# Performance work log

Measured on AMD Instinct MI355X. Metric: run time of the kernel, lower is better.

The kernel has to match this reference:

```python
import jax, jax.numpy as jnp
import numpy as np

N, E = 20000, 320000
IN, H, C = 1024, 8, 64
HC = H * C
EDGE_DIM = 16
NUM_GRAPHS = 8
LEAKY_SLOPE = 0.2
LN_EPS = 1e-5


def setup_inputs() -> dict:
    key = jax.random.key(0)
    ks = jax.random.split(key, 12)
    s = 0.05
    return {
        "x": jax.random.normal(ks[0], (N, IN), jnp.float32),
        "edge_attr": jax.random.normal(ks[1], (E, EDGE_DIM), jnp.float32),
        "edge_index": jax.random.randint(ks[2], (2, E), 0, N, dtype=jnp.int64),
        "batch": jnp.sort(jax.random.randint(ks[3], (N,), 0, NUM_GRAPHS, dtype=jnp.int64)),
        "W_src": jax.random.normal(ks[4], (IN, HC), jnp.float32) * s,
        "W_dst": jax.random.normal(ks[5], (IN, HC), jnp.float32) * s,
        "att_src": jax.random.normal(ks[6], (H, C), jnp.float32) * s,
        "att_dst": jax.random.normal(ks[7], (H, C), jnp.float32) * s,
        "bias": jnp.zeros((HC,), jnp.float32),
        "ln_gamma": jnp.ones((HC,), jnp.float32),
        "ln_beta": jnp.zeros((HC,), jnp.float32),
        "prelu_a": jnp.full((HC,), 0.25, jnp.float32),
    }


def reference(x, edge_attr, edge_index, batch, W_src, W_dst, att_src, att_dst,
              bias, ln_gamma, ln_beta, prelu_a):
    # Eval mode: node/edge feature dropout and attention dropout are identity.
    # with_edge == 'N': edge_attr is unused by the conv.
    n = x.shape[0]
    src, dst = edge_index[0], edge_index[1]

    xs = (x @ W_src).reshape(n, H, C)   # source-side projections
    xd = (x @ W_dst).reshape(n, H, C)   # dest-side projections
    a_src = jnp.einsum('nhc,hc->nh', xs, att_src)
    a_dst = jnp.einsum('nhc,hc->nh', xd, att_dst)

    # edge scores + softmax over incoming edges of each destination node
    e = jax.nn.leaky_relu(a_src[src] + a_dst[dst], LEAKY_SLOPE)  # [E,H]
    m = jax.ops.segment_max(e, dst, num_segments=n)              # [N,H]
    m = jax.lax.stop_gradient(jnp.where(jnp.isfinite(m), m, 0.0))
    ex = jnp.exp(e - m[dst])
    denom = jax.ops.segment_sum(ex, dst, num_segments=n)
    alpha = ex / (denom[dst] + 1e-16)                            # [E,H]

    msg = alpha[:, :, None] * xs[src]                            # [E,H,C]
    out = jax.ops.segment_sum(msg, dst, num_segments=n).reshape(n, HC) + bias

    # norm_type == 'layer': the per-graph boolean-mask loop applies LayerNorm
    # row-wise; with sorted batch ids this equals a single LayerNorm over all
    # nodes (LayerNorm has no cross-row statistics).
    mu = jnp.mean(out, axis=-1, keepdims=True)
    var = jnp.mean(jnp.square(out - mu), axis=-1, keepdims=True)
    y = (out - mu) * jax.lax.rsqrt(var + LN_EPS) * ln_gamma + ln_beta

    # PReLU with per-channel slope
    return jnp.where(y >= 0, y, prelu_a * y)
```

## Files before the change

kernel.cpp:

```cpp
#include <hip/hip_runtime.h>
#include <hip/hip_bf16.h>

#define N_NODES 20000
#define N_EDGES 320000
#define IN_DIM  1024
#define H_HEADS 8
#define C_CH    64
#define HC      512
#define LEAKY   0.2f
#define LN_EPS  1e-5f

#define BCOLS 576

typedef short bf16x8 __attribute__((ext_vector_type(8)));
typedef float f32x4  __attribute__((ext_vector_type(4)));

__device__ __forceinline__ unsigned short f2bf(float f) {
    union { float f; unsigned int u; } c; c.f = f;
    unsigned int u = c.u;
    unsigned int r = (u + 0x7fffu + ((u >> 16) & 1u)) >> 16;
    return (unsigned short)r;
}
__device__ __forceinline__ float bf2f(unsigned int h) {
    union { unsigned int u; float f; } c; c.u = h << 16; return c.f;
}
__device__ __forceinline__ unsigned int bfpack(float lo, float hi) {
    return (unsigned int)f2bf(lo) | ((unsigned int)f2bf(hi) << 16);
}
__device__ __forceinline__ void gload_lds16(const void* g, void* l) {
    __builtin_amdgcn_global_load_lds(
        (const __attribute__((address_space(1))) unsigned int*)g,
        (__attribute__((address_space(3))) unsigned int*)l, 16, 0, 0);
}

#define DEG_BLOCKS 1250

__global__ __launch_bounds__(256) void deg_hist(
        const int* __restrict__ ei, int* __restrict__ deg) {
    int e = blockIdx.x * 256 + threadIdx.x;
    atomicAdd(&deg[ei[N_EDGES + e]], 1);
}

__global__ void prep_w_scan(const float* __restrict__ Wsrc,
                            const float* __restrict__ Wdst,
                            const float* __restrict__ att_src,
                            const float* __restrict__ att_dst,
                            short* __restrict__ wbT,
                            const int* __restrict__ deg,
                            int* __restrict__ off,
                            int* __restrict__ cursor) {
    int t = threadIdx.x;

    if (blockIdx.x == IN_DIM) {
        __shared__ int wtot[2];
        int lane = t & 63, w = t >> 6;
        const int4* deg4 = (const int4*)deg;
        int s = 0;
        if (t < 125) {
            #pragma unroll
            for (int j = 0; j < 40; ++j) {
                int4 u = deg4[t * 40 + j];
                s += u.x + u.y + u.z + u.w;
            }
        }
        int v = s;
        #pragma unroll
        for (int o = 1; o < 64; o <<= 1) {
            int u = __shfl_up(v, o);
            if (lane >= o) v += u;
        }
        if (lane == 63) wtot[w] = v;
        __syncthreads();
        int add = (w == 1) ? wtot[0] : 0;
        int run = add + v - s;
        if (t < 125) {
            int4* off4 = (int4*)off;
            int4* cur4 = (int4*)cursor;
            #pragma unroll
            for (int j = 0; j < 40; ++j) {
                int4 u = deg4[t * 40 + j];
                int4 o_;
                o_.x = run;
                o_.y = o_.x + u.x;
                o_.z = o_.y + u.y;
                o_.w = o_.z + u.z;
                off4[t * 40 + j] = o_;
                cur4[t * 40 + j] = o_;
                run = o_.w + u.w;
            }
            if (t == 124) off[N_NODES] = run;
        }
        return;
    }

    int k = blockIdx.x;
    float4 v = *(const float4*)(Wsrc + (size_t)k * HC + t * 4);
    wbT[(size_t)(t * 4 + 0) * IN_DIM + k] = (short)f2bf(v.x);
    wbT[(size_t)(t * 4 + 1) * IN_DIM + k] = (short)f2bf(v.y);
    wbT[(size_t)(t * 4 + 2) * IN_DIM + k] = (short)f2bf(v.z);
    wbT[(size_t)(t * 4 + 3) * IN_DIM + k] = (short)f2bf(v.w);
    if (t < 16) {
        int h = t & 7;
        const float* W   = (t < 8) ? Wsrc : Wdst;
        const float* att = (t < 8) ? att_src : att_dst;
        float s = 0.f;
        #pragma unroll
        for (int c = 0; c < C_CH; ++c)
            s += W[(size_t)k * HC + h * C_CH + c] * att[h * C_CH + c];
        wbT[(size_t)(512 + t) * IN_DIM + k] = (short)f2bf(s);
    } else if (t < 64) {
        wbT[(size_t)(512 + t) * IN_DIM + k] = 0;
    }
}

#define BM 64
#define BN 96
#define BK 64
#define NCOLT (BCOLS / BN)
#define NROWT ((N_NODES + BM - 1) / BM)
#define NWG (NCOLT * NROWT)
#define KSTEPS (IN_DIM / BK)
#define A_SLOTS (BM * BK / 8)
#define B_SLOTS (BN * BK / 8)

__global__ __launch_bounds__(256) void gemm_scatter(
        const float* __restrict__ x,
        const short* __restrict__ wbT,
        short* __restrict__ xsb,
        float* __restrict__ a_srcv,
        float* __restrict__ a_dstv,
        const int* __restrict__ ei,
        int* __restrict__ cursor,
        int* __restrict__ csr_src) {
    __shared__ short As[A_SLOTS * 8];
    __shared__ short Bs[B_SLOTS * 8];

    int t = threadIdx.x;

    if (blockIdx.x >= NWG) {
        int e = (blockIdx.x - NWG) * 256 + t;
        int d = ei[N_EDGES + e];
        int idx = atomicAdd(&cursor[d], 1);
        csr_src[idx] = ei[e];
        return;
    }

    int orig = blockIdx.x;
    const int q = NWG >> 3, r = NWG & 7;
    int xcd  = orig & 7;
    int wgid = (xcd < r ? xcd * (q + 1) : r * (q + 1) + (xcd - r) * q) + (orig >> 3);
    int col0 = (wgid % NCOLT) * BN;
    int row0 = (wgid / NCOLT) * BM;

    int lane = t & 63;
    int w    = t >> 6;
    int lr   = lane & 15;
    int lg   = lane >> 4;
    int sw   = lr & 7;
    int wr   = (w >> 1) * 32;
    int wc   = (w & 1) * 48;

    const float* a_base[2];
    #pragma unroll
    for (int i = 0; i < 2; ++i) {
        int s  = t + 256 * i;
        int m  = s >> 3;
        int kc = (s & 7) ^ (m & 7);
        int gm = row0 + m;
        if (gm >= N_NODES) gm = N_NODES - 1;
        a_base[i] = x + (size_t)gm * IN_DIM + kc * 8;
    }
    const short* b_base[3];
    #pragma unroll
    for (int i = 0; i < 3; ++i) {
        int s  = t + 256 * i;
        int c  = s >> 3;
        int kc = (s & 7) ^ (c & 7);
        b_base[i] = wbT + (size_t)(col0 + c) * IN_DIM + kc * 8;
    }

    f32x4 acc[2][3] = {};

    for (int step = 0; step < KSTEPS; ++step) {
        int k0 = step * BK;
        #pragma unroll
        for (int i = 0; i < 2; ++i) {
            float4 fa = *(const float4*)(a_base[i] + k0);
            float4 fb = *(const float4*)(a_base[i] + k0 + 4);
            uint4 rr;
            rr.x = bfpack(fa.x, fa.y);
            rr.y = bfpack(fa.z, fa.w);
            rr.z = bfpack(fb.x, fb.y);
            rr.w = bfpack(fb.z, fb.w);
            *(uint4*)(&As[(t + 256 * i) * 8]) = rr;
        }
        #pragma unroll
        for (int i = 0; i < 3; ++i)
            gload_lds16(b_base[i] + k0, &Bs[(t + 256 * i) * 8]);
        __syncthreads();

        #pragma unroll
        for (int ks = 0; ks < 2; ++ks) {
            int kc  = ks * 4 + lg;
            int kca = kc ^ sw;
            bf16x8 af[2], bfr[3];
            #pragma unroll
            for (int mi = 0; mi < 2; ++mi)
                af[mi] = *(const bf16x8*)(&As[((wr + mi * 16 + lr) * 8 + kca) * 8]);
            #pragma unroll
            for (int ni = 0; ni < 3; ++ni)
                bfr[ni] = *(const bf16x8*)(&Bs[((wc + ni * 16 + lr) * 8 + kca) * 8]);
            __builtin_amdgcn_s_setprio(1);
            #pragma unroll
            for (int mi = 0; mi < 2; ++mi)
                #pragma unroll
                for (int ni = 0; ni < 3; ++ni)
                    acc[mi][ni] = __builtin_amdgcn_mfma_f32_16x16x32_bf16(
                        af[mi], bfr[ni], acc[mi][ni], 0, 0, 0);
            __builtin_amdgcn_s_setprio(0);
        }
        __syncthreads();
    }

    #pragma unroll
    for (int mi = 0; mi < 2; ++mi) {
        #pragma unroll
        for (int rr = 0; rr < 4; ++rr) {
            int row = row0 + wr + mi * 16 + lg * 4 + rr;
            if (row >= N_NODES) continue;
            #pragma unroll
            for (int ni = 0; ni < 3; ++ni) {
                int col = col0 + wc + ni * 16 + lr;
                float v = acc[mi][ni][rr];
                if (col < 512)      xsb[(size_t)row * HC + col] = (short)f2bf(v);
                else if (col < 520) a_srcv[(size_t)row * 8 + (col - 512)] = v;
                else if (col < 528) a_dstv[(size_t)row * 8 + (col - 520)] = v;
            }
        }
    }
}

__global__ __launch_bounds__(256) void aggregate_ln(
        const int* __restrict__ off,
        const int* __restrict__ csr_src,
        const float* __restrict__ a_srcv,
        const float* __restrict__ a_dstv,
        const short* __restrict__ xsb,
        const float* __restrict__ bias,
        const float* __restrict__ gamma,
        const float* __restrict__ beta,
        const float* __restrict__ prelu_a,
        float* __restrict__ out) {
    int lane = threadIdx.x & 63;
    int n    = blockIdx.x * 4 + (threadIdx.x >> 6);
    int ch0  = lane * 8;
    int h    = lane >> 3;

    int start = off[n], end = off[n + 1];
    float ad  = a_dstv[(size_t)n * 8 + h];

    float acc[8] = {};
    float wsum = 0.f;

    int i = start;
    for (; i + 1 < end; i += 2) {
        int s0 = __builtin_amdgcn_readfirstlane(csr_src[i]);
        int s1 = __builtin_amdgcn_readfirstlane(csr_src[i + 1]);
        float sc0 = a_srcv[(size_t)s0 * 8 + h] + ad;
        float sc1 = a_srcv[(size_t)s1 * 8 + h] + ad;
        uint4 u0 = *(const uint4*)(xsb + (size_t)s0 * HC + ch0);
        uint4 u1 = *(const uint4*)(xsb + (size_t)s1 * HC + ch0);
        sc0 = (sc0 >= 0.f) ? sc0 : LEAKY * sc0;
        sc1 = (sc1 >= 0.f) ? sc1 : LEAKY * sc1;
        float w0 = __expf(sc0);
        float w1 = __expf(sc1);
        acc[0] = fmaf(w0, bf2f(u0.x & 0xffffu), acc[0]);
        acc[1] = fmaf(w0, bf2f(u0.x >> 16),     acc[1]);
        acc[2] = fmaf(w0, bf2f(u0.y & 0xffffu), acc[2]);
        acc[3] = fmaf(w0, bf2f(u0.y >> 16),     acc[3]);
        acc[4] = fmaf(w0, bf2f(u0.z & 0xffffu), acc[4]);
        acc[5] = fmaf(w0, bf2f(u0.z >> 16),     acc[5]);
        acc[6] = fmaf(w0, bf2f(u0.w & 0xffffu), acc[6]);
        acc[7] = fmaf(w0, bf2f(u0.w >> 16),     acc[7]);
        acc[0] = fmaf(w1, bf2f(u1.x & 0xffffu), acc[0]);
        acc[1] = fmaf(w1, bf2f(u1.x >> 16),     acc[1]);
        acc[2] = fmaf(w1, bf2f(u1.y & 0xffffu), acc[2]);
        acc[3] = fmaf(w1, bf2f(u1.y >> 16),     acc[3]);
        acc[4] = fmaf(w1, bf2f(u1.z & 0xffffu), acc[4]);
        acc[5] = fmaf(w1, bf2f(u1.z >> 16),     acc[5]);
        acc[6] = fmaf(w1, bf2f(u1.w & 0xffffu), acc[6]);
        acc[7] = fmaf(w1, bf2f(u1.w >> 16),     acc[7]);
        wsum += w0 + w1;
    }
    if (i < end) {
        int s0 = __builtin_amdgcn_readfirstlane(csr_src[i]);
        float sc0 = a_srcv[(size_t)s0 * 8 + h] + ad;
        uint4 u0 = *(const uint4*)(xsb + (size_t)s0 * HC + ch0);
        sc0 = (sc0 >= 0.f) ? sc0 : LEAKY * sc0;
        float w0 = __expf(sc0);
        acc[0] = fmaf(w0, bf2f(u0.x & 0xffffu), acc[0]);
        acc[1] = fmaf(w0, bf2f(u0.x >> 16),     acc[1]);
        acc[2] = fmaf(w0, bf2f(u0.y & 0xffffu), acc[2]);
        acc[3] = fmaf(w0, bf2f(u0.y >> 16),     acc[3]);
        acc[4] = fmaf(w0, bf2f(u0.z & 0xffffu), acc[4]);
        acc[5] = fmaf(w0, bf2f(u0.z >> 16),     acc[5]);
        acc[6] = fmaf(w0, bf2f(u0.w & 0xffffu), acc[6]);
        acc[7] = fmaf(w0, bf2f(u0.w >> 16),     acc[7]);
        wsum += w0;
    }

    float inv = 1.f / (wsum + 1e-16f);
    float4 b0 = *(const float4*)(bias + ch0);
    float4 b1 = *(const float4*)(bias + ch0 + 4);
    float v8[8];
    float psum = 0.f, psq = 0.f;
    const float bb[8] = {b0.x, b0.y, b0.z, b0.w, b1.x, b1.y, b1.z, b1.w};
    #pragma unroll
    for (int j = 0; j < 8; ++j) {
        v8[j] = acc[j] * inv + bb[j];
        psum += v8[j];
        psq  += v8[j] * v8[j];
    }
    #pragma unroll
    for (int o = 32; o > 0; o >>= 1) {
        psum += __shfl_xor(psum, o);
        psq  += __shfl_xor(psq, o);
    }
    float mu   = psum * (1.f / (float)HC);
    float var  = psq * (1.f / (float)HC) - mu * mu;
    float rstd = rsqrtf(var + LN_EPS);

    float4 g0 = *(const float4*)(gamma + ch0);
    float4 g1 = *(const float4*)(gamma + ch0 + 4);
    float4 e0 = *(const float4*)(beta + ch0);
    float4 e1 = *(const float4*)(beta + ch0 + 4);
    float4 p0 = *(const float4*)(prelu_a + ch0);
    float4 p1 = *(const float4*)(prelu_a + ch0 + 4);
    const float gg[8] = {g0.x, g0.y, g0.z, g0.w, g1.x, g1.y, g1.z, g1.w};
    const float ee[8] = {e0.x, e0.y, e0.z, e0.w, e1.x, e1.y, e1.z, e1.w};
    const float pp[8] = {p0.x, p0.y, p0.z, p0.w, p1.x, p1.y, p1.z, p1.w};
    float y[8];
    #pragma unroll
    for (int j = 0; j < 8; ++j) {
        float v = (v8[j] - mu) * rstd * gg[j] + ee[j];
        y[j] = (v >= 0.f) ? v : pp[j] * v;
    }
    float4* o4 = (float4*)(out + (size_t)n * HC + ch0);
    o4[0] = make_float4(y[0], y[1], y[2], y[3]);
    o4[1] = make_float4(y[4], y[5], y[6], y[7]);
}

extern "C" void kernel_launch(void* const* d_in, const int* in_sizes, int n_in,
                              void* d_out, int out_size, void* d_ws, size_t ws_size,
                              hipStream_t stream) {
    const float* x        = (const float*)d_in[0];
    const int*   ei       = (const int*)d_in[2];
    const float* Wsrc     = (const float*)d_in[4];
    const float* Wdst     = (const float*)d_in[5];
    const float* att_src  = (const float*)d_in[6];
    const float* att_dst  = (const float*)d_in[7];
    const float* bias     = (const float*)d_in[8];
    const float* gamma    = (const float*)d_in[9];
    const float* beta     = (const float*)d_in[10];
    const float* prelu_a  = (const float*)d_in[11];
    float* out            = (float*)d_out;

    char*  ws = (char*)d_ws;
    size_t o  = 0;
    auto alloc = [&](size_t bytes) -> void* {
        void* p = ws + o;
        o += (bytes + 255) & ~(size_t)255;
        return p;
    };
    short* wbT     = (short*)alloc(sizeof(short) * BCOLS * IN_DIM);
    short* xsb     = (short*)alloc(sizeof(short) * (size_t)N_NODES * HC);
    float* a_srcv  = (float*)alloc(sizeof(float) * N_NODES * 8);
    float* a_dstv  = (float*)alloc(sizeof(float) * N_NODES * 8);
    int*   deg     = (int*)alloc(sizeof(int) * N_NODES);
    int*   off     = (int*)alloc(sizeof(int) * (N_NODES + 1));
    int*   cursor  = (int*)alloc(sizeof(int) * N_NODES);
    int*   csr_src = (int*)alloc(sizeof(int) * N_EDGES);

    hipMemsetAsync(deg, 0, sizeof(int) * N_NODES, stream);

    deg_hist<<<DEG_BLOCKS, 256, 0, stream>>>(ei, deg);

    prep_w_scan<<<IN_DIM + 1, 128, 0, stream>>>(Wsrc, Wdst, att_src, att_dst,
                                                wbT, deg, off, cursor);

    gemm_scatter<<<NWG + DEG_BLOCKS, 256, 0, stream>>>(
        x, wbT, xsb, a_srcv, a_dstv, ei, cursor, csr_src);

    aggregate_ln<<<N_NODES / 4, 256, 0, stream>>>(
        off, csr_src, a_srcv, a_dstv, xsb, bias, gamma, beta, prelu_a, out);
}
```

Before: 148.0 us.

## Double-buffer GEMM LDS tiles and use hardware bf16 pack conversion

```diff
diff --git a/kernel.cpp b/kernel.cpp
--- a/kernel.cpp
+++ b/kernel.cpp
@@ -24,8 +24,10 @@
 __device__ __forceinline__ float bf2f(unsigned int h) {
     union { unsigned int u; float f; } c; c.u = h << 16; return c.f;
 }
-__device__ __forceinline__ unsigned int bfpack(float lo, float hi) {
-    return (unsigned int)f2bf(lo) | ((unsigned int)f2bf(hi) << 16);
+__device__ __forceinline__ unsigned int cvtpk(float lo, float hi) {
+    unsigned int r;
+    asm("v_cvt_pk_bf16_f32 %0, %1, %2" : "=v"(r) : "v"(lo), "v"(hi));
+    return r;
 }
 __device__ __forceinline__ void gload_lds16(const void* g, void* l) {
     __builtin_amdgcn_global_load_lds(
@@ -132,8 +134,8 @@
         const int* __restrict__ ei,
         int* __restrict__ cursor,
         int* __restrict__ csr_src) {
-    __shared__ short As[A_SLOTS * 8];
-    __shared__ short Bs[B_SLOTS * 8];
+    __shared__ short As[2][A_SLOTS * 8];
+    __shared__ short Bs[2][B_SLOTS * 8];
 
     int t = threadIdx.x;
 
@@ -181,46 +183,79 @@
 
     f32x4 acc[2][3] = {};
 
-    for (int step = 0; step < KSTEPS; ++step) {
-        int k0 = step * BK;
-        #pragma unroll
-        for (int i = 0; i < 2; ++i) {
-            float4 fa = *(const float4*)(a_base[i] + k0);
-            float4 fb = *(const float4*)(a_base[i] + k0 + 4);
-            uint4 rr;
-            rr.x = bfpack(fa.x, fa.y);
-            rr.y = bfpack(fa.z, fa.w);
-            rr.z = bfpack(fb.x, fb.y);
-            rr.w = bfpack(fb.z, fb.w);
-            *(uint4*)(&As[(t + 256 * i) * 8]) = rr;
-        }
+#define A_WRITE(buf, fa0, fb0, fa1, fb1)                                      \
+    do {                                                                      \
+        uint4 r0, r1;                                                         \
+        r0.x = cvtpk(fa0.x, fa0.y);  r0.y = cvtpk(fa0.z, fa0.w);              \
+        r0.z = cvtpk(fb0.x, fb0.y);  r0.w = cvtpk(fb0.z, fb0.w);              \
+        r1.x = cvtpk(fa1.x, fa1.y);  r1.y = cvtpk(fa1.z, fa1.w);              \
+        r1.z = cvtpk(fb1.x, fb1.y);  r1.w = cvtpk(fb1.z, fb1.w);              \
+        *(uint4*)(&As[buf][(t      ) * 8]) = r0;                              \
+        *(uint4*)(&As[buf][(t + 256) * 8]) = r1;                              \
+    } while (0)
+
+#define COMPUTE(buf)                                                          \
+    do {                                                                      \
+        _Pragma("unroll")                                                     \
+        for (int ks = 0; ks < 2; ++ks) {                                      \
+            int kc  = ks * 4 + lg;                                            \
+            int kca = kc ^ sw;                                                \
+            bf16x8 af[2], bfr[3];                                             \
+            _Pragma("unroll")                                                 \
+            for (int mi = 0; mi < 2; ++mi)                                    \
+                af[mi] = *(const bf16x8*)(&As[buf][((wr + mi * 16 + lr) * 8 + kca) * 8]); \
+            _Pragma("unroll")                                                 \
+            for (int ni = 0; ni < 3; ++ni)                                    \
+                bfr[ni] = *(const bf16x8*)(&Bs[buf][((wc + ni * 16 + lr) * 8 + kca) * 8]); \
+            __builtin_amdgcn_s_setprio(1);                                    \
+            _Pragma("unroll")                                                 \
+            for (int mi = 0; mi < 2; ++mi)                                    \
+                _Pragma("unroll")                                             \
+                for (int ni = 0; ni < 3; ++ni)                                \
+                    acc[mi][ni] = __builtin_amdgcn_mfma_f32_16x16x32_bf16(    \
+                        af[mi], bfr[ni], acc[mi][ni], 0, 0, 0);               \
+            __builtin_amdgcn_s_setprio(0);                                    \
+        }                                                                     \
+    } while (0)
+
+    {
+        float4 fa0 = *(const float4*)(a_base[0]);
+        float4 fb0 = *(const float4*)(a_base[0] + 4);
+        float4 fa1 = *(const float4*)(a_base[1]);
+        float4 fb1 = *(const float4*)(a_base[1] + 4);
         #pragma unroll
         for (int i = 0; i < 3; ++i)
-            gload_lds16(b_base[i] + k0, &Bs[(t + 256 * i) * 8]);
-        __syncthreads();
-
-        #pragma unroll
-        for (int ks = 0; ks < 2; ++ks) {
-            int kc  = ks * 4 + lg;
-            int kca = kc ^ sw;
-            bf16x8 af[2], bfr[3];
+            gload_lds16(b_base[i], &Bs[0][(t + 256 * i) * 8]);
+        A_WRITE(0, fa0, fb0, fa1, fb1);
+        asm volatile("s_waitcnt vmcnt(0) lgkmcnt(0)" ::: "memory");
+        __builtin_amdgcn_s_barrier();
+    }
+
+    int cur = 0;
+    for (int step = 0; step < KSTEPS; ++step) {
+        float4 fa0, fb0, fa1, fb1;
+        if (step + 1 < KSTEPS) {
+            int k1 = (step + 1) * BK;
+            fa0 = *(const float4*)(a_base[0] + k1);
+            fb0 = *(const float4*)(a_base[0] + k1 + 4);
+            fa1 = *(const float4*)(a_base[1] + k1);
+            fb1 = *(const float4*)(a_base[1] + k1 + 4);
             #pragma unroll
-            for (int mi = 0; mi < 2; ++mi)
-                af[mi] = *(const bf16x8*)(&As[((wr + mi * 16 + lr) * 8 + kca) * 8]);
-            #pragma unroll
-            for (int ni = 0; ni < 3; ++ni)
-                bfr[ni] = *(const bf16x8*)(&Bs[((wc + ni * 16 + lr) * 8 + kca) * 8]);
-            __builtin_amdgcn_s_setprio(1);
-            #pragma unroll
-            for (int mi = 0; mi < 2; ++mi)
-                #pragma unroll
-                for (int ni = 0; ni < 3; ++ni)
-                    acc[mi][ni] = __builtin_amdgcn_mfma_f32_16x16x32_bf16(
-                        af[mi], bfr[ni], acc[mi][ni], 0, 0, 0);
-            __builtin_amdgcn_s_setprio(0);
+            for (int i = 0; i < 3; ++i)
+                gload_lds16(b_base[i] + k1, &Bs[cur ^ 1][(t + 256 * i) * 8]);
         }
-        __syncthreads();
-    }
+
+        COMPUTE(cur);
+
+        if (step + 1 < KSTEPS)
+            A_WRITE(cur ^ 1, fa0, fb0, fa1, fb1);
+
+        asm volatile("s_waitcnt vmcnt(0) lgkmcnt(0)" ::: "memory");
+        __builtin_amdgcn_s_barrier();
+        cur ^= 1;
+    }
+#undef A_WRITE
+#undef COMPUTE
 
     #pragma unroll
     for (int mi = 0; mi < 2; ++mi) {
```

After: 147.6 us. About the same (-0.2%).

## Pre-pack x and W into MFMA fragment layout, drop LDS staging in GEMM

Applied to the files above, without the earlier changes.

```diff
diff --git a/kernel.cpp b/kernel.cpp
--- a/kernel.cpp
+++ b/kernel.cpp
@@ -11,6 +11,10 @@
 #define LN_EPS  1e-5f
 
 #define BCOLS 576
+#define NCT   36
+#define NKT   32
+#define NRT   1250
+
 
 typedef short bf16x8 __attribute__((ext_vector_type(8)));
 typedef float f32x4  __attribute__((ext_vector_type(4)));
@@ -24,36 +28,116 @@
 __device__ __forceinline__ float bf2f(unsigned int h) {
     union { unsigned int u; float f; } c; c.u = h << 16; return c.f;
 }
-__device__ __forceinline__ unsigned int bfpack(float lo, float hi) {
-    return (unsigned int)f2bf(lo) | ((unsigned int)f2bf(hi) << 16);
-}
-__device__ __forceinline__ void gload_lds16(const void* g, void* l) {
-    __builtin_amdgcn_global_load_lds(
-        (const __attribute__((address_space(1))) unsigned int*)g,
-        (__attribute__((address_space(3))) unsigned int*)l, 16, 0, 0);
+__device__ __forceinline__ unsigned int cvtpk(float lo, float hi) {
+    unsigned int r;
+    asm("v_cvt_pk_bf16_f32 %0, %1, %2" : "=v"(r) : "v"(lo), "v"(hi));
+    return r;
 }
 
 #define DEG_BLOCKS 1250
-
-__global__ __launch_bounds__(256) void deg_hist(
-        const int* __restrict__ ei, int* __restrict__ deg) {
-    int e = blockIdx.x * 256 + threadIdx.x;
-    atomicAdd(&deg[ei[N_EDGES + e]], 1);
-}
-
-__global__ void prep_w_scan(const float* __restrict__ Wsrc,
-                            const float* __restrict__ Wdst,
-                            const float* __restrict__ att_src,
-                            const float* __restrict__ att_dst,
-                            short* __restrict__ wbT,
-                            const int* __restrict__ deg,
-                            int* __restrict__ off,
-                            int* __restrict__ cursor) {
+#define CONV_BLOCKS NRT
+#define PREP_BLOCKS NKT
+
+__global__ __launch_bounds__(256) void fused_pre(
+        const float* __restrict__ x,
+        const int* __restrict__ ei,
+        const float* __restrict__ Wsrc,
+        const float* __restrict__ Wdst,
+        const float* __restrict__ att_src,
+        const float* __restrict__ att_dst,
+        short* __restrict__ xbt,
+        short* __restrict__ wbtt,
+        int* __restrict__ deg) {
+    __shared__ short sw[32 * 512];
+    __shared__ float f1[32][8], f2[32][8];
+    int t   = threadIdx.x;
+    int bid = blockIdx.x;
+
+    if (bid < DEG_BLOCKS) {
+        int e = bid * 256 + t;
+        atomicAdd(&deg[ei[N_EDGES + e]], 1);
+        return;
+    }
+
+    if (bid < DEG_BLOCKS + CONV_BLOCKS) {
+        int rt   = bid - DEG_BLOCKS;
+        int lane = t & 63, w = t >> 6;
+        int lr = lane & 15, lg = lane >> 4;
+        const float* xr = x + (size_t)(rt * 16 + lr) * IN_DIM;
+        #pragma unroll
+        for (int i = 0; i < 8; ++i) {
+            int kt = w + i * 4;
+            float4 f = *(const float4*)(xr + kt * 32 + lg * 8);
+            float4 g = *(const float4*)(xr + kt * 32 + lg * 8 + 4);
+            uint4 r;
+            r.x = cvtpk(f.x, f.y);  r.y = cvtpk(f.z, f.w);
+            r.z = cvtpk(g.x, g.y);  r.w = cvtpk(g.z, g.w);
+            *(uint4*)(xbt + (((size_t)rt * 32 + kt) << 9) + lane * 8) = r;
+        }
+        return;
+    }
+
+    int kt = bid - (DEG_BLOCKS + CONV_BLOCKS);
+    int k0 = kt * 32;
+    for (int i = t; i < 32 * 128; i += 256) {
+        int kk = i >> 7, g4 = i & 127;
+        float4 v = *(const float4*)(Wsrc + (size_t)(k0 + kk) * HC + g4 * 4);
+        uint2 p;
+        p.x = cvtpk(v.x, v.y);  p.y = cvtpk(v.z, v.w);
+        *(uint2*)(&sw[kk * 512 + g4 * 4]) = p;
+    }
+    {
+        int kk = t >> 3, h = t & 7;
+        const float* wsr = Wsrc + (size_t)(k0 + kk) * HC + h * 64;
+        const float* wdr = Wdst + (size_t)(k0 + kk) * HC + h * 64;
+        const float* a1  = att_src + h * 64;
+        const float* a2  = att_dst + h * 64;
+        float s1 = 0.f, s2 = 0.f;
+        #pragma unroll 8
+        for (int c = 0; c < 64; ++c) {
+            s1 += wsr[c] * a1[c];
+            s2 += wdr[c] * a2[c];
+        }
+        f1[kk][h] = s1;  f2[kk][h] = s2;
+    }
+    __syncthreads();
+    for (int idx = t; idx < NCT * 64; idx += 256) {
+        int ct = idx >> 6, sl = idx & 63;
+        int lr = sl & 15, lg = sl >> 4;
+        int col = ct * 16 + lr;
+        union { short v[8]; uint4 u; } pk;
+        #pragma unroll
+        for (int j = 0; j < 8; ++j) {
+            int kk = lg * 8 + j;
+            short val;
+            if (col < 512)      val = sw[kk * 512 + col];
+            else if (col < 520) val = (short)f2bf(f1[kk][col - 512]);
+            else if (col < 528) val = (short)f2bf(f2[kk][col - 520]);
+            else                val = 0;
+            pk.v[j] = val;
+        }
+        *(uint4*)(wbtt + (((size_t)ct * 32 + kt) << 9) + sl * 8) = pk.u;
+    }
+}
+
+#define NCOLT 6
+#define NROWT 313
+#define NWG (NROWT * NCOLT)
+
+__global__ __launch_bounds__(256) void gemm_scan(
+        const short* __restrict__ xbt,
+        const short* __restrict__ wbtt,
+        short* __restrict__ xsb,
+        float* __restrict__ a_srcv,
+        float* __restrict__ a_dstv,
+        const int* __restrict__ deg,
+        int* __restrict__ off,
+        int* __restrict__ cursor) {
     int t = threadIdx.x;
 
-    if (blockIdx.x == IN_DIM) {
+    if (blockIdx.x == NWG) {
         __shared__ int wtot[2];
-        int lane = t & 63, w = t >> 6;
+        int lane = t & 63, wv = t >> 6;
         const int4* deg4 = (const int4*)deg;
         int s = 0;
         if (t < 125) {
@@ -69,9 +153,9 @@
             int u = __shfl_up(v, o);
             if (lane >= o) v += u;
         }
-        if (lane == 63) wtot[w] = v;
+        if (lane == 63 && wv < 2) wtot[wv] = v;
         __syncthreads();
-        int add = (w == 1) ? wtot[0] : 0;
+        int add = (wv == 1) ? wtot[0] : 0;
         int run = add + v - s;
         if (t < 125) {
             int4* off4 = (int4*)off;
@@ -93,144 +177,52 @@
         return;
     }
 
-    int k = blockIdx.x;
-    float4 v = *(const float4*)(Wsrc + (size_t)k * HC + t * 4);
-    wbT[(size_t)(t * 4 + 0) * IN_DIM + k] = (short)f2bf(v.x);
-    wbT[(size_t)(t * 4 + 1) * IN_DIM + k] = (short)f2bf(v.y);
-    wbT[(size_t)(t * 4 + 2) * IN_DIM + k] = (short)f2bf(v.z);
-    wbT[(size_t)(t * 4 + 3) * IN_DIM + k] = (short)f2bf(v.w);
-    if (t < 16) {
-        int h = t & 7;
-        const float* W   = (t < 8) ? Wsrc : Wdst;
-        const float* att = (t < 8) ? att_src : att_dst;
-        float s = 0.f;
-        #pragma unroll
-        for (int c = 0; c < C_CH; ++c)
-            s += W[(size_t)k * HC + h * C_CH + c] * att[h * C_CH + c];
-        wbT[(size_t)(512 + t) * IN_DIM + k] = (short)f2bf(s);
-    } else if (t < 64) {
-        wbT[(size_t)(512 + t) * IN_DIM + k] = 0;
-    }
-}
-
-#define BM 64
-#define BN 96
-#define BK 64
-#define NCOLT (BCOLS / BN)
-#define NROWT ((N_NODES + BM - 1) / BM)
-#define NWG (NCOLT * NROWT)
-#define KSTEPS (IN_DIM / BK)
-#define A_SLOTS (BM * BK / 8)
-#define B_SLOTS (BN * BK / 8)
-
-__global__ __launch_bounds__(256) void gemm_scatter(
-        const float* __restrict__ x,
-        const short* __restrict__ wbT,
-        short* __restrict__ xsb,
-        float* __restrict__ a_srcv,
-        float* __restrict__ a_dstv,
-        const int* __restrict__ ei,
-        int* __restrict__ cursor,
-        int* __restrict__ csr_src) {
-    __shared__ short As[A_SLOTS * 8];
-    __shared__ short Bs[B_SLOTS * 8];
-
-    int t = threadIdx.x;
-
-    if (blockIdx.x >= NWG) {
-        int e = (blockIdx.x - NWG) * 256 + t;
-        int d = ei[N_EDGES + e];
-        int idx = atomicAdd(&cursor[d], 1);
-        csr_src[idx] = ei[e];
-        return;
-    }
-
     int orig = blockIdx.x;
     const int q = NWG >> 3, r = NWG & 7;
     int xcd  = orig & 7;
     int wgid = (xcd < r ? xcd * (q + 1) : r * (q + 1) + (xcd - r) * q) + (orig >> 3);
-    int col0 = (wgid % NCOLT) * BN;
-    int row0 = (wgid / NCOLT) * BM;
+    int colblk = wgid % NCOLT;
+    int rowblk = wgid / NCOLT;
+    int row0 = (rowblk < NROWT - 1) ? rowblk * 64 : (N_NODES - 64);
 
     int lane = t & 63;
     int w    = t >> 6;
     int lr   = lane & 15;
     int lg   = lane >> 4;
-    int sw   = lr & 7;
-    int wr   = (w >> 1) * 32;
-    int wc   = (w & 1) * 48;
-
-    const float* a_base[2];
-    #pragma unroll
-    for (int i = 0; i < 2; ++i) {
-        int s  = t + 256 * i;
-        int m  = s >> 3;
-        int kc = (s & 7) ^ (m & 7);
-        int gm = row0 + m;
-        if (gm >= N_NODES) gm = N_NODES - 1;
-        a_base[i] = x + (size_t)gm * IN_DIM + kc * 8;
-    }
-    const short* b_base[3];
-    #pragma unroll
-    for (int i = 0; i < 3; ++i) {
-        int s  = t + 256 * i;
-        int c  = s >> 3;
-        int kc = (s & 7) ^ (c & 7);
-        b_base[i] = wbT + (size_t)(col0 + c) * IN_DIM + kc * 8;
-    }
+    int rtw  = (row0 >> 4) + (w >> 1) * 2;
+    int ctw  = colblk * 6 + (w & 1) * 3;
+
+    const short* pa0 = xbt  + (((size_t)(rtw + 0) * 32) << 9) + lane * 8;
+    const short* pa1 = xbt  + (((size_t)(rtw + 1) * 32) << 9) + lane * 8;
+    const short* pb0 = wbtt + (((size_t)(ctw + 0) * 32) << 9) + lane * 8;
+    const short* pb1 = wbtt + (((size_t)(ctw + 1) * 32) << 9) + lane * 8;
+    const short* pb2 = wbtt + (((size_t)(ctw + 2) * 32) << 9) + lane * 8;
 
     f32x4 acc[2][3] = {};
 
-    for (int step = 0; step < KSTEPS; ++step) {
-        int k0 = step * BK;
-        #pragma unroll
-        for (int i = 0; i < 2; ++i) {
-            float4 fa = *(const float4*)(a_base[i] + k0);
-            float4 fb = *(const float4*)(a_base[i] + k0 + 4);
-            uint4 rr;
-            rr.x = bfpack(fa.x, fa.y);
-            rr.y = bfpack(fa.z, fa.w);
-            rr.z = bfpack(fb.x, fb.y);
-            rr.w = bfpack(fb.z, fb.w);
-            *(uint4*)(&As[(t + 256 * i) * 8]) = rr;
-        }
-        #pragma unroll
-        for (int i = 0; i < 3; ++i)
-            gload_lds16(b_base[i] + k0, &Bs[(t + 256 * i) * 8]);
-        __syncthreads();
-
-        #pragma unroll
-        for (int ks = 0; ks < 2; ++ks) {
-            int kc  = ks * 4 + lg;
-            int kca = kc ^ sw;
-            bf16x8 af[2], bfr[3];
-            #pragma unroll
-            for (int mi = 0; mi < 2; ++mi)
-                af[mi] = *(const bf16x8*)(&As[((wr + mi * 16 + lr) * 8 + kca) * 8]);
-            #pragma unroll
-            for (int ni = 0; ni < 3; ++ni)
-                bfr[ni] = *(const bf16x8*)(&Bs[((wc + ni * 16 + lr) * 8 + kca) * 8]);
-            __builtin_amdgcn_s_setprio(1);
-            #pragma unroll
-            for (int mi = 0; mi < 2; ++mi)
-                #pragma unroll
-                for (int ni = 0; ni < 3; ++ni)
-                    acc[mi][ni] = __builtin_amdgcn_mfma_f32_16x16x32_bf16(
-                        af[mi], bfr[ni], acc[mi][ni], 0, 0, 0);
-            __builtin_amdgcn_s_setprio(0);
-        }
-        __syncthreads();
+    #pragma unroll 4
+    for (int kt = 0; kt < NKT; ++kt) {
+        bf16x8 a0 = *(const bf16x8*)(pa0 + kt * 512);
+        bf16x8 a1 = *(const bf16x8*)(pa1 + kt * 512);
+        bf16x8 b0 = *(const bf16x8*)(pb0 + kt * 512);
+        bf16x8 b1 = *(const bf16x8*)(pb1 + kt * 512);
+        bf16x8 b2 = *(const bf16x8*)(pb2 + kt * 512);
+        acc[0][0] = __builtin_amdgcn_mfma_f32_16x16x32_bf16(a0, b0, acc[0][0], 0, 0, 0);
+        acc[0][1] = __builtin_amdgcn_mfma_f32_16x16x32_bf16(a0, b1, acc[0][1], 0, 0, 0);
+        acc[0][2] = __builtin_amdgcn_mfma_f32_16x16x32_bf16(a0, b2, acc[0][2], 0, 0, 0);
+        acc[1][0] = __builtin_amdgcn_mfma_f32_16x16x32_bf16(a1, b0, acc[1][0], 0, 0, 0);
+        acc[1][1] = __builtin_amdgcn_mfma_f32_16x16x32_bf16(a1, b1, acc[1][1], 0, 0, 0);
+        acc[1][2] = __builtin_amdgcn_mfma_f32_16x16x32_bf16(a1, b2, acc[1][2], 0, 0, 0);
     }
 
     #pragma unroll
     for (int mi = 0; mi < 2; ++mi) {
         #pragma unroll
         for (int rr = 0; rr < 4; ++rr) {
-            int row = row0 + wr + mi * 16 + lg * 4 + rr;
-            if (row >= N_NODES) continue;
+            int row = (rtw + mi) * 16 + lg * 4 + rr;
             #pragma unroll
             for (int ni = 0; ni < 3; ++ni) {
-                int col = col0 + wc + ni * 16 + lr;
+                int col = (ctw + ni) * 16 + lr;
                 float v = acc[mi][ni][rr];
                 if (col < 512)      xsb[(size_t)row * HC + col] = (short)f2bf(v);
                 else if (col < 520) a_srcv[(size_t)row * 8 + (col - 512)] = v;
@@ -238,6 +230,16 @@
             }
         }
     }
+}
+
+__global__ __launch_bounds__(256) void edge_scatter(
+        const int* __restrict__ ei,
+        int* __restrict__ cursor,
+        int* __restrict__ csr_src) {
+    int e = blockIdx.x * 256 + threadIdx.x;
+    int d = ei[N_EDGES + e];
+    int idx = atomicAdd(&cursor[d], 1);
+    csr_src[idx] = ei[e];
 }
 
 __global__ __launch_bounds__(256) void aggregate_ln(
@@ -372,7 +374,7 @@
         o += (bytes + 255) & ~(size_t)255;
         return p;
     };
-    short* wbT     = (short*)alloc(sizeof(short) * BCOLS * IN_DIM);
+    short* wbtt    = (short*)alloc(sizeof(short) * NCT * NKT * 512);
     short* xsb     = (short*)alloc(sizeof(short) * (size_t)N_NODES * HC);
     float* a_srcv  = (float*)alloc(sizeof(float) * N_NODES * 8);
     float* a_dstv  = (float*)alloc(sizeof(float) * N_NODES * 8);
@@ -381,15 +383,17 @@
     int*   cursor  = (int*)alloc(sizeof(int) * N_NODES);
     int*   csr_src = (int*)alloc(sizeof(int) * N_EDGES);
 
+    short* xbt = (short*)d_out;
+
     hipMemsetAsync(deg, 0, sizeof(int) * N_NODES, stream);
 
-    deg_hist<<<DEG_BLOCKS, 256, 0, stream>>>(ei, deg);
-
-    prep_w_scan<<<IN_DIM + 1, 128, 0, stream>>>(Wsrc, Wdst, att_src, att_dst,
-                                                wbT, deg, off, cursor);
-
-    gemm_scatter<<<NWG + DEG_BLOCKS, 256, 0, stream>>>(
-        x, wbT, xsb, a_srcv, a_dstv, ei, cursor, csr_src);
+    fused_pre<<<DEG_BLOCKS + CONV_BLOCKS + PREP_BLOCKS, 256, 0, stream>>>(
+        x, ei, Wsrc, Wdst, att_src, att_dst, xbt, wbtt, deg);
+
+    gemm_scan<<<NWG + 1, 256, 0, stream>>>(
+        xbt, wbtt, xsb, a_srcv, a_dstv, deg, off, cursor);
+
+    edge_scatter<<<N_EDGES / 256, 256, 0, stream>>>(ei, cursor, csr_src);
 
     aggregate_ln<<<N_NODES / 4, 256, 0, stream>>>(
         off, csr_src, a_srcv, a_dstv, xsb, bias, gamma, beta, prelu_a, out);
```

Result: slower. 174.5 us (+17.9%).
